# Optimization experiments

Hardware: AMD Instinct MI355X
Metric: run time of the kernel (lower is better)

## Reference

```python
import jax, jax.numpy as jnp
import numpy as np

BS, NUM_RELS, NUM_NODES, EMB = 8, 16, 512, 256


def setup_inputs() -> dict:
    key = jax.random.key(0)
    k1, k2, k3, k4 = jax.random.split(key, 4)
    features = jax.random.normal(k1, (BS, NUM_NODES, EMB), dtype=jnp.float32)
    adjacency = jax.random.uniform(k2, (BS, NUM_RELS, NUM_NODES, NUM_NODES), dtype=jnp.float32)
    # xavier_uniform bounds
    bound = float(np.sqrt(6.0 / (EMB + EMB)))
    W_r = jax.random.uniform(k3, (NUM_RELS, EMB, EMB), minval=-bound, maxval=bound, dtype=jnp.float32)
    W_0 = jax.random.uniform(k4, (EMB, EMB), minval=-bound, maxval=bound, dtype=jnp.float32)
    return {"features": features, "adjacency": adjacency, "W_r": W_r, "W_0": W_0}


def reference(features, adjacency, W_r, W_0):
    # msg[b,r,n,d] = sum_m adjacency[b,r,n,m] * features[b,m,d]
    msg = jnp.einsum('brnm,bmd->brnd', adjacency, features)
    # per-relation projection then sum over relations: [b,n,h]
    features_1 = jnp.einsum('brnd,rdh->bnh', msg, W_r)
    features_2 = jnp.einsum('bnd,dh->bnh', features, W_0)
    return jax.nn.relu(features_1 + features_2)
```

## Files before the change

kernel.cpp:

```cpp
#include <hip/hip_runtime.h>
#include <hip/hip_bf16.h>

#define BS   8
#define NREL 16
#define NN   512
#define EMB  256

typedef float f32x4 __attribute__((ext_vector_type(4)));
typedef short s16x8 __attribute__((ext_vector_type(8)));

__device__ __forceinline__ unsigned short f2bf_bits(float f) {
    union { float f; unsigned u; } v; v.f = f;
    unsigned r = (v.u + 0x7FFFu + ((v.u >> 16) & 1u)) >> 16;
    return (unsigned short)r;
}

__device__ __forceinline__ unsigned short f2bf_hw(float f) {
    union { __hip_bfloat16 h; unsigned short u; } v;
    v.h = __float2bfloat16(f);
    return v.u;
}

__global__ __launch_bounds__(256) void k0_prep(
        const float* __restrict__ Wr, const float* __restrict__ W0,
        const float* __restrict__ F,
        unsigned short* __restrict__ wT, unsigned short* __restrict__ Fbf) {
    int bid = blockIdx.x;
    if (bid < 1088) {
        __shared__ float tile[32][33];
        int rel = bid / 64;
        int t   = bid % 64;
        int d0  = (t & 7) * 32;
        int h0  = (t >> 3) * 32;
        int tx  = threadIdx.x & 31;
        int ty  = threadIdx.x >> 5;
        const float* src = (rel < NREL) ? (Wr + rel * (EMB * EMB)) : W0;
#pragma unroll
        for (int k = 0; k < 4; ++k) {
            int d = d0 + ty + k * 8;
            tile[ty + k * 8][tx] = src[d * EMB + h0 + tx];
        }
        __syncthreads();
#pragma unroll
        for (int k = 0; k < 4; ++k) {
            int h = h0 + ty + k * 8;
            wT[(rel * EMB + h) * EMB + d0 + tx] = f2bf_bits(tile[tx][ty + k * 8]);
        }
    } else {
        long i = ((long)(bid - 1088) * 256 + threadIdx.x) * 8;
        f32x4 x0 = *(const f32x4*)(F + i);
        f32x4 x1 = *(const f32x4*)(F + i + 4);
        s16x8 v;
        v[0] = (short)f2bf_bits(x0[0]); v[1] = (short)f2bf_bits(x0[1]);
        v[2] = (short)f2bf_bits(x0[2]); v[3] = (short)f2bf_bits(x0[3]);
        v[4] = (short)f2bf_bits(x1[0]); v[5] = (short)f2bf_bits(x1[1]);
        v[6] = (short)f2bf_bits(x1[2]); v[7] = (short)f2bf_bits(x1[3]);
        *(s16x8*)(Fbf + i) = v;
    }
}

__global__ __launch_bounds__(256) void k1_fw(
        const unsigned short* __restrict__ Fbf, const unsigned short* __restrict__ wT,
        unsigned short* __restrict__ FW, float* __restrict__ F2f) {
    int bid = blockIdx.x;
    int b   = bid & 7;
    int q   = bid >> 3;
    int rel = q % 17;
    int mt  = q / 17;
    int tid = threadIdx.x;
    int w   = tid >> 6;
    int l   = tid & 63;
    int lg  = l >> 4;
    int lr  = l & 15;

    int h0 = w * 64;
    int m0 = mt * 64;

    const unsigned short* wt = wT + rel * (EMB * EMB) + lg * 8;
    const unsigned short* Fb = Fbf + (long)b * (NN * EMB) + lg * 8;

    f32x4 acc[4][4];
#pragma unroll
    for (int i = 0; i < 4; ++i)
#pragma unroll
        for (int j = 0; j < 4; ++j) acc[i][j] = (f32x4){0.f, 0.f, 0.f, 0.f};

    s16x8 afr[2][4], bfr[2][4];
#pragma unroll
    for (int hi = 0; hi < 4; ++hi)
        afr[0][hi] = *(const s16x8*)(wt + (h0 + hi * 16 + lr) * EMB);
#pragma unroll
    for (int bi = 0; bi < 4; ++bi)
        bfr[0][bi] = *(const s16x8*)(Fb + (m0 + bi * 16 + lr) * EMB);

#pragma unroll
    for (int kk = 0; kk < 8; ++kk) {
        int cur = kk & 1, nxt = cur ^ 1;
        if (kk < 7) {
            int ko = (kk + 1) * 32;
#pragma unroll
            for (int hi = 0; hi < 4; ++hi)
                afr[nxt][hi] = *(const s16x8*)(wt + (h0 + hi * 16 + lr) * EMB + ko);
#pragma unroll
            for (int bi = 0; bi < 4; ++bi)
                bfr[nxt][bi] = *(const s16x8*)(Fb + (m0 + bi * 16 + lr) * EMB + ko);
        }
#pragma unroll
        for (int hi = 0; hi < 4; ++hi)
#pragma unroll
            for (int bi = 0; bi < 4; ++bi)
                acc[hi][bi] = __builtin_amdgcn_mfma_f32_16x16x32_bf16(
                    afr[cur][hi], bfr[cur][bi], acc[hi][bi], 0, 0, 0);
    }

#pragma unroll
    for (int hi = 0; hi < 4; ++hi) {
#pragma unroll
        for (int bi = 0; bi < 4; ++bi) {
            int m  = m0 + bi * 16 + lr;
            int kg = m >> 3, ko = m & 7;
#pragma unroll
            for (int j = 0; j < 4; ++j) {
                int h = h0 + hi * 16 + lg * 4 + j;
                if (rel < NREL)
                    FW[(long)((b * 16 + rel) * 64 + kg) * 2048 + h * 8 + ko] =
                        f2bf_bits(acc[hi][bi][j]);
                else
                    F2f[((long)b * NN + m) * EMB + h] = acc[hi][bi][j];
            }
        }
    }
}

__global__ __launch_bounds__(512, 2) void k2_main(
        const float* __restrict__ adj, const unsigned short* __restrict__ FW,
        float* __restrict__ part) {
    __shared__ unsigned short Blds[2][16384];
    int bid = blockIdx.x;
    int b   = bid & 7;
    int t   = bid >> 3;
    int nt  = t & 3;
    int rg  = t >> 2;
    int tid = threadIdx.x;
    int w   = tid >> 6;
    int l   = tid & 63;
    int lg  = l >> 4, lr = l & 15;
    int wr  = w >> 1;
    int wc  = w & 1;

    int nrow = nt * 128 + wr * 32;

    f32x4 acc0[16], acc1[16];
#pragma unroll
    for (int i = 0; i < 16; ++i) {
        acc0[i] = (f32x4){0.f, 0.f, 0.f, 0.f};
        acc1[i] = (f32x4){0.f, 0.f, 0.f, 0.f};
    }

    const float* adjb0 =
        adj + (((long)(b * 16 + rg * 2)) * NN + nrow + lr) * NN + lg * 8;
    const float* adjb1 = adjb0 + 16 * NN;
    const unsigned short* fwb = FW + (long)(b * 16 + rg * 2) * 131072;

    s16x8 fwr[4];
    f32x4 ax[2][2], ay[2][2];

#define POFF(p) ((long)((p) >> 3) * 131072 + ((p) & 7) * 16384)

    {
        const unsigned short* s = fwb + POFF(0) + tid * 8;
#pragma unroll
        for (int c = 0; c < 4; ++c) fwr[c] = *(const s16x8*)(s + c * 4096);
#pragma unroll
        for (int c = 0; c < 4; ++c)
            *(s16x8*)(&Blds[0][c * 4096 + tid * 8]) = fwr[c];
    }
    {
        const float* p0 = adjb0 + wc * 32;
        const float* p1 = adjb1 + wc * 32;
        ax[0][0] = *(const f32x4*)p0; ay[0][0] = *(const f32x4*)(p0 + 4);
        ax[0][1] = *(const f32x4*)p1; ay[0][1] = *(const f32x4*)(p1 + 4);
    }
    {
        const unsigned short* s = fwb + POFF(1) + tid * 8;
#pragma unroll
        for (int c = 0; c < 4; ++c) fwr[c] = *(const s16x8*)(s + c * 4096);
    }
    asm volatile("s_waitcnt lgkmcnt(0)" ::: "memory");
    __builtin_amdgcn_sched_barrier(0);
    __builtin_amdgcn_s_barrier();
    asm volatile("" ::: "memory");

#pragma unroll
    for (int i = 0; i < 16; ++i) {
        if (i + 1 < 16) {
            int sl = 2 * (i + 1) + wc;
            long ao = (long)(sl >> 4) * (NN * NN) + (sl & 15) * 32;
            const float* p0 = adjb0 + ao;
            const float* p1 = adjb1 + ao;
            if (((i + 1) & 1) == 0) {
                ax[0][0] = *(const f32x4*)p0; ay[0][0] = *(const f32x4*)(p0 + 4);
                ax[0][1] = *(const f32x4*)p1; ay[0][1] = *(const f32x4*)(p1 + 4);
            } else {
                ax[1][0] = *(const f32x4*)p0; ay[1][0] = *(const f32x4*)(p0 + 4);
                ax[1][1] = *(const f32x4*)p1; ay[1][1] = *(const f32x4*)(p1 + 4);
            }
        }

        f32x4 x00 = ax[i & 1][0], x01 = ay[i & 1][0];
        f32x4 x10 = ax[i & 1][1], x11 = ay[i & 1][1];
        s16x8 a0, a1;
        a0[0] = (short)f2bf_hw(x00[0]); a0[1] = (short)f2bf_hw(x00[1]);
        a0[2] = (short)f2bf_hw(x00[2]); a0[3] = (short)f2bf_hw(x00[3]);
        a0[4] = (short)f2bf_hw(x01[0]); a0[5] = (short)f2bf_hw(x01[1]);
        a0[6] = (short)f2bf_hw(x01[2]); a0[7] = (short)f2bf_hw(x01[3]);
        a1[0] = (short)f2bf_hw(x10[0]); a1[1] = (short)f2bf_hw(x10[1]);
        a1[2] = (short)f2bf_hw(x10[2]); a1[3] = (short)f2bf_hw(x10[3]);
        a1[4] = (short)f2bf_hw(x11[0]); a1[5] = (short)f2bf_hw(x11[1]);
        a1[6] = (short)f2bf_hw(x11[2]); a1[7] = (short)f2bf_hw(x11[3]);

        const unsigned short* bl = &Blds[i & 1][wc * 8192 + lg * 2048];
#pragma unroll
        for (int f = 0; f < 16; ++f) {
            s16x8 bf = *(const s16x8*)(bl + (f * 16 + lr) * 8);
            acc0[f] = __builtin_amdgcn_mfma_f32_16x16x32_bf16(a0, bf, acc0[f], 0, 0, 0);
            acc1[f] = __builtin_amdgcn_mfma_f32_16x16x32_bf16(a1, bf, acc1[f], 0, 0, 0);
        }
        asm volatile("" ::: "memory");

        if (i + 1 < 16) {
            unsigned short* dst = &Blds[(i + 1) & 1][tid * 8];
#pragma unroll
            for (int c = 0; c < 4; ++c) *(s16x8*)(dst + c * 4096) = fwr[c];
            if (i + 2 < 16) {
                const unsigned short* s = fwb + POFF(i + 2) + tid * 8;
#pragma unroll
                for (int c = 0; c < 4; ++c) fwr[c] = *(const s16x8*)(s + c * 4096);
            }
            asm volatile("s_waitcnt lgkmcnt(0)" ::: "memory");
            __builtin_amdgcn_sched_barrier(0);
            __builtin_amdgcn_s_barrier();
            asm volatile("" ::: "memory");
        }
    }
#undef POFF

    float* lf = (float*)Blds;
    float* pp = part + ((long)rg * BS + b) * (NN * EMB);
#pragma unroll
    for (int g = 0; g < 2; ++g) {
        __syncthreads();
        if (wc == 1) {
#pragma unroll
            for (int f = 0; f < 16; ++f)
#pragma unroll
                for (int j = 0; j < 4; ++j)
                    lf[wr * 4096 + (f * 4 + j) * 64 + l] =
                        g ? acc1[f][j] : acc0[f][j];
        }
        __syncthreads();
        if (wc == 0) {
#pragma unroll
            for (int f = 0; f < 16; ++f) {
                int h = f * 16 + lr;
#pragma unroll
                for (int j = 0; j < 4; ++j) {
                    int n = nrow + g * 16 + lg * 4 + j;
                    float v = (g ? acc1[f][j] : acc0[f][j]) +
                              lf[wr * 4096 + (f * 4 + j) * 64 + l];
                    pp[(long)n * EMB + h] = v;
                }
            }
        }
    }
}

__global__ __launch_bounds__(256) void k3_reduce(
        const float* __restrict__ part, const float* __restrict__ F2f,
        float* __restrict__ out) {
    const long PS = (long)BS * NN * EMB;
    long i = ((long)blockIdx.x * 256 + threadIdx.x) * 4;
    f32x4 s = *(const f32x4*)(part + i);
#pragma unroll
    for (int rg = 1; rg < 8; ++rg)
        s += *(const f32x4*)(part + i + (long)rg * PS);
    s += *(const f32x4*)(F2f + i);
    f32x4 r;
#pragma unroll
    for (int j = 0; j < 4; ++j) r[j] = s[j] > 0.f ? s[j] : 0.f;
    *(f32x4*)(out + i) = r;
}

extern "C" void kernel_launch(void* const* d_in, const int* in_sizes, int n_in,
                              void* d_out, int out_size, void* d_ws, size_t ws_size,
                              hipStream_t stream) {
    const float* F   = (const float*)d_in[0];
    const float* adj = (const float*)d_in[1];
    const float* Wr  = (const float*)d_in[2];
    const float* W0  = (const float*)d_in[3];
    float* out = (float*)d_out;

    unsigned short* wT  = (unsigned short*)d_ws;
    unsigned short* Fbf = wT + 17 * 256 * 256;
    unsigned short* FW  = Fbf + (long)8 * 512 * 256;
    float* F2f  = (float*)(FW + (long)8 * 16 * 64 * 2048);
    float* part = F2f + (long)8 * 512 * 256;

    k0_prep<<<1600, 256, 0, stream>>>(Wr, W0, F, wT, Fbf);
    k1_fw<<<1088, 256, 0, stream>>>(Fbf, wT, FW, F2f);
    k2_main<<<256, 512, 0, stream>>>(adj, FW, part);
    k3_reduce<<<1024, 256, 0, stream>>>(part, F2f, out);
}
```

Measured before the change: 99.09 us.

## Retile k2_main warps to 64 rows by 128 columns for better LDS reuse

Each warp now computes 4 row fragments of 16 rows across 8 output column fragments, half of the H dimension, instead of 2 row fragments across all 16 column fragments. Each B fragment read from LDS feeds 4 MFMAs instead of 2, which halves LDS reads per MFMA. In exchange each lane converts twice as many adjacency values to bf16 and issues twice as many global loads per step. The same adjacency data is now loaded redundantly by the two H-halves, raising global traffic and register pressure. The epilogue is reindexed to match the new fragment layout.

```diff
diff --git a/kernel.cpp b/kernel.cpp
--- a/kernel.cpp
+++ b/kernel.cpp
@@ -145,25 +145,25 @@
     int w   = tid >> 6;
     int l   = tid & 63;
     int lg  = l >> 4, lr = l & 15;
-    int wr  = w >> 1;
     int wc  = w & 1;
-
-    int nrow = nt * 128 + wr * 32;
-
-    f32x4 acc0[16], acc1[16];
-#pragma unroll
-    for (int i = 0; i < 16; ++i) {
-        acc0[i] = (f32x4){0.f, 0.f, 0.f, 0.f};
-        acc1[i] = (f32x4){0.f, 0.f, 0.f, 0.f};
-    }
-
-    const float* adjb0 =
-        adj + (((long)(b * 16 + rg * 2)) * NN + nrow + lr) * NN + lg * 8;
-    const float* adjb1 = adjb0 + 16 * NN;
+    int hh  = (w >> 1) & 1;
+    int rh  = w >> 2;
+
+    int nrow0 = nt * 128 + rh * 64;
+    int h0    = hh * 128;
+
+    f32x4 acc[4][8];
+#pragma unroll
+    for (int ar = 0; ar < 4; ++ar)
+#pragma unroll
+        for (int f = 0; f < 8; ++f) acc[ar][f] = (f32x4){0.f, 0.f, 0.f, 0.f};
+
+    const float* adjb =
+        adj + (((long)(b * 16 + rg * 2)) * NN + nrow0 + lr) * NN + lg * 8;
     const unsigned short* fwb = FW + (long)(b * 16 + rg * 2) * 131072;
 
     s16x8 fwr[4];
-    f32x4 ax[2][2], ay[2][2];
+    f32x4 ax[2][4], ay[2][4];
 
 #define POFF(p) ((long)((p) >> 3) * 131072 + ((p) & 7) * 16384)
 
@@ -176,10 +176,12 @@
             *(s16x8*)(&Blds[0][c * 4096 + tid * 8]) = fwr[c];
     }
     {
-        const float* p0 = adjb0 + wc * 32;
-        const float* p1 = adjb1 + wc * 32;
-        ax[0][0] = *(const f32x4*)p0; ay[0][0] = *(const f32x4*)(p0 + 4);
-        ax[0][1] = *(const f32x4*)p1; ay[0][1] = *(const f32x4*)(p1 + 4);
+#pragma unroll
+        for (int ar = 0; ar < 4; ++ar) {
+            const float* p = adjb + ar * (16 * NN) + wc * 32;
+            ax[0][ar] = *(const f32x4*)p;
+            ay[0][ar] = *(const f32x4*)(p + 4);
+        }
     }
     {
         const unsigned short* s = fwb + POFF(1) + tid * 8;
@@ -196,35 +198,37 @@
         if (i + 1 < 16) {
             int sl = 2 * (i + 1) + wc;
             long ao = (long)(sl >> 4) * (NN * NN) + (sl & 15) * 32;
-            const float* p0 = adjb0 + ao;
-            const float* p1 = adjb1 + ao;
-            if (((i + 1) & 1) == 0) {
-                ax[0][0] = *(const f32x4*)p0; ay[0][0] = *(const f32x4*)(p0 + 4);
-                ax[0][1] = *(const f32x4*)p1; ay[0][1] = *(const f32x4*)(p1 + 4);
-            } else {
-                ax[1][0] = *(const f32x4*)p0; ay[1][0] = *(const f32x4*)(p0 + 4);
-                ax[1][1] = *(const f32x4*)p1; ay[1][1] = *(const f32x4*)(p1 + 4);
+#pragma unroll
+            for (int ar = 0; ar < 4; ++ar) {
+                const float* p = adjb + ar * (16 * NN) + ao;
+                if (((i + 1) & 1) == 0) {
+                    ax[0][ar] = *(const f32x4*)p; ay[0][ar] = *(const f32x4*)(p + 4);
+                } else {
+                    ax[1][ar] = *(const f32x4*)p; ay[1][ar] = *(const f32x4*)(p + 4);
+                }
             }
         }
 
-        f32x4 x00 = ax[i & 1][0], x01 = ay[i & 1][0];
-        f32x4 x10 = ax[i & 1][1], x11 = ay[i & 1][1];
-        s16x8 a0, a1;
-        a0[0] = (short)f2bf_hw(x00[0]); a0[1] = (short)f2bf_hw(x00[1]);
-        a0[2] = (short)f2bf_hw(x00[2]); a0[3] = (short)f2bf_hw(x00[3]);
-        a0[4] = (short)f2bf_hw(x01[0]); a0[5] = (short)f2bf_hw(x01[1]);
-        a0[6] = (short)f2bf_hw(x01[2]); a0[7] = (short)f2bf_hw(x01[3]);
-        a1[0] = (short)f2bf_hw(x10[0]); a1[1] = (short)f2bf_hw(x10[1]);
-        a1[2] = (short)f2bf_hw(x10[2]); a1[3] = (short)f2bf_hw(x10[3]);
-        a1[4] = (short)f2bf_hw(x11[0]); a1[5] = (short)f2bf_hw(x11[1]);
-        a1[6] = (short)f2bf_hw(x11[2]); a1[7] = (short)f2bf_hw(x11[3]);
+        s16x8 afr[4];
+#pragma unroll
+        for (int ar = 0; ar < 4; ++ar) {
+            f32x4 x0 = ax[i & 1][ar], x1 = ay[i & 1][ar];
+            s16x8 a;
+            a[0] = (short)f2bf_hw(x0[0]); a[1] = (short)f2bf_hw(x0[1]);
+            a[2] = (short)f2bf_hw(x0[2]); a[3] = (short)f2bf_hw(x0[3]);
+            a[4] = (short)f2bf_hw(x1[0]); a[5] = (short)f2bf_hw(x1[1]);
+            a[6] = (short)f2bf_hw(x1[2]); a[7] = (short)f2bf_hw(x1[3]);
+            afr[ar] = a;
+        }
 
         const unsigned short* bl = &Blds[i & 1][wc * 8192 + lg * 2048];
 #pragma unroll
-        for (int f = 0; f < 16; ++f) {
-            s16x8 bf = *(const s16x8*)(bl + (f * 16 + lr) * 8);
-            acc0[f] = __builtin_amdgcn_mfma_f32_16x16x32_bf16(a0, bf, acc0[f], 0, 0, 0);
-            acc1[f] = __builtin_amdgcn_mfma_f32_16x16x32_bf16(a1, bf, acc1[f], 0, 0, 0);
+        for (int f = 0; f < 8; ++f) {
+            s16x8 bf = *(const s16x8*)(bl + (h0 + f * 16 + lr) * 8);
+            acc[0][f] = __builtin_amdgcn_mfma_f32_16x16x32_bf16(afr[0], bf, acc[0][f], 0, 0, 0);
+            acc[1][f] = __builtin_amdgcn_mfma_f32_16x16x32_bf16(afr[1], bf, acc[1][f], 0, 0, 0);
+            acc[2][f] = __builtin_amdgcn_mfma_f32_16x16x32_bf16(afr[2], bf, acc[2][f], 0, 0, 0);
+            acc[3][f] = __builtin_amdgcn_mfma_f32_16x16x32_bf16(afr[3], bf, acc[3][f], 0, 0, 0);
         }
         asm volatile("" ::: "memory");
 
@@ -247,28 +251,35 @@
 
     float* lf = (float*)Blds;
     float* pp = part + ((long)rg * BS + b) * (NN * EMB);
+    int wid2 = w >> 1;
 #pragma unroll
     for (int g = 0; g < 2; ++g) {
         __syncthreads();
         if (wc == 1) {
 #pragma unroll
-            for (int f = 0; f < 16; ++f)
-#pragma unroll
-                for (int j = 0; j < 4; ++j)
-                    lf[wr * 4096 + (f * 4 + j) * 64 + l] =
-                        g ? acc1[f][j] : acc0[f][j];
+            for (int aq = 0; aq < 2; ++aq)
+#pragma unroll
+                for (int f = 0; f < 8; ++f)
+#pragma unroll
+                    for (int j = 0; j < 4; ++j)
+                        lf[wid2 * 4096 + ((aq * 8 + f) * 4 + j) * 64 + l] =
+                            acc[g * 2 + aq][f][j];
         }
         __syncthreads();
         if (wc == 0) {
 #pragma unroll
-            for (int f = 0; f < 16; ++f) {
-                int h = f * 16 + lr;
-#pragma unroll
-                for (int j = 0; j < 4; ++j) {
-                    int n = nrow + g * 16 + lg * 4 + j;
-                    float v = (g ? acc1[f][j] : acc0[f][j]) +
-                              lf[wr * 4096 + (f * 4 + j) * 64 + l];
-                    pp[(long)n * EMB + h] = v;
+            for (int aq = 0; aq < 2; ++aq) {
+                int ar = g * 2 + aq;
+#pragma unroll
+                for (int f = 0; f < 8; ++f) {
+                    int h = h0 + f * 16 + lr;
+#pragma unroll
+                    for (int j = 0; j < 4; ++j) {
+                        int n = nrow0 + ar * 16 + lg * 4 + j;
+                        float v = acc[ar][f][j] +
+                                  lf[wid2 * 4096 + ((aq * 8 + f) * 4 + j) * 64 + l];
+                        pp[(long)n * EMB + h] = v;
+                    }
                 }
             }
         }
```

New measurement: 110.2 us. +11.2%, slower.
